# Kernel optimization log

Measured on AMD Instinct MI355X. Metric: run time of the kernel, lower is better.

## Reference

```python
import jax, jax.numpy as jnp
import numpy as np

A0, A1, A2 = 1.0, 1.0, 0.5  # Taylor coefficients of exp around 0 (p=2)

B, H, N, D = 2, 16, 4096, 32


def setup_inputs() -> dict:
    key = jax.random.key(0)
    kq, kk, kv = jax.random.split(key, 3)
    q = jax.random.normal(kq, (B, H, N, D), dtype=jnp.float32)
    k = jax.random.normal(kk, (B, H, N, D), dtype=jnp.float32)
    v = jax.random.normal(kv, (B, H, N, D), dtype=jnp.float32)
    return {"q": q, "k": k, "v": v}


def reference(q, k, v):
    # fastmax_function with p=2, mask=False, normalize=False, dropout=0 -> temperature=1
    b, h, n, d = q.shape
    # quadratic feature maps: flatten of outer products, [b,h,n,d*d]
    q2 = (q[..., :, None] * q[..., None, :]).reshape(b, h, n, d * d)
    k2 = (k[..., :, None] * k[..., None, :]).reshape(b, h, n, d * d)
    # numerator: a0*sum(v) + a1*q(k^T v) + a2*q2(k2^T v)
    second_term = A1 * jnp.einsum('bhnd,bhne->bhde', k, v)           # [b,h,d,d]
    third_term = A2 * jnp.einsum('bhnf,bhne->bhfe', k2, v)           # [b,h,d^2,d]
    ans = (jnp.einsum('bhnd,bhde->bhne', q, second_term)
           + jnp.einsum('bhnf,bhfe->bhne', q2, third_term)
           + A0 * jnp.sum(v, axis=-2, keepdims=True))                 # [b,h,n,d]
    # denominator: a0*n + a1*q.sum(k) + a2*q2.sum(k2)
    div = (A0 * n
           + A1 * jnp.einsum('bhnd,bhd->bhn', q, jnp.sum(k, axis=-2))
           + A2 * jnp.einsum('bhnf,bhf->bhn', q2, jnp.sum(k2, axis=-2)))  # [b,h,n]
    return ans / div[..., None]
```

## Files before the change

kernel.cpp:

```cpp
#include <hip/hip_runtime.h>

#define NTOK 4096
#define NBH  32
#define NF   576
#define NE   33
#define NKT  18
#define GTF_BH (NKT * 3 * 64 * 8)
#define GTF_HALF (9 * 3 * 64 * 8)
#define KC   16
#define NSTG 2
#define NVB  (KC * NBH)
#define NP8  (NBH * NE * NF / 8)

typedef _Float16 half_t;
typedef _Float16 half8 __attribute__((ext_vector_type(8)));
typedef _Float16 half4v __attribute__((ext_vector_type(4)));
typedef float f32x4 __attribute__((ext_vector_type(4)));
typedef unsigned int u32;

#define MFMA16(A,B,C) __builtin_amdgcn_mfma_f32_16x16x32_f16((A),(B),(C),0,0,0)

#define ASYNC_CP16(dst_lds, src_glb) \
    __builtin_amdgcn_global_load_lds( \
        (const __attribute__((address_space(1))) u32*)(const void*)(src_glb), \
        (__attribute__((address_space(3))) u32*)(void*)(dst_lds), 16, 0, 0)

static __device__ __forceinline__ half8 splat8(half_t x) {
    return (half8){x, x, x, x, x, x, x, x};
}

static __device__ __forceinline__ int FS(int d) { return (d + (d >> 3)) & 15; }

__global__ __launch_bounds__(256, 2)
void ta_kernel(const float* __restrict__ kin, const float* __restrict__ vin,
               half_t* __restrict__ P)
{
    __shared__ __align__(16) half_t kb0[2 * 4096];
    __shared__ __align__(16) half_t vb0[2 * 4096];

    const int vb = blockIdx.x;
    const int bh = vb & (NBH - 1), kc = vb >> 5;
    const int t = threadIdx.x;
    const int w = t >> 6, lane = t & 63, l16 = lane & 15, quad = lane >> 4;
    const int pw = w * 144;
    const half8 h05 = splat8((half_t)0.5f);

    f32x4 acc[9][3];
    #pragma unroll
    for (int m = 0; m < 9; ++m)
        #pragma unroll
        for (int e = 0; e < 3; ++e)
            acc[m][e] = (f32x4){0.f, 0.f, 0.f, 0.f};

    int rotoff[9], rotsalt[9];
    #pragma unroll
    for (int mt = 0; mt < 9; ++mt) {
        const int pm = pw + mt * 16;
        int ro = 0, rs = 0;
        if (pm >= 32 && pm < 512) {
            const int s  = 1 + ((pm - 32) >> 5);
            const int i0 = (pm - 32) & 31;
            const int r  = (i0 + l16 + s) & 31;
            ro = r * 128;
            rs = FS(r);
        }
        rotoff[mt] = ro;
        rotsalt[mt] = rs;
    }
    const int sh0 = FS(l16), sh1 = FS(l16 + 16);

    const size_t fbase = ((size_t)bh * NTOK + kc * 256) * 32;
    const float4* k4 = (const float4*)kin + fbase / 4;
    const float4* v4 = (const float4*)vin + fbase / 4;

    float kaf[16], vaf[16];
    auto loadst = [&](int s) {
        const int base = s * 1024;
        #pragma unroll
        for (int r = 0; r < 4; ++r) {
            float4 kk = k4[base + t + 256 * r];
            float4 vv = v4[base + t + 256 * r];
            kaf[4*r+0] = kk.x; kaf[4*r+1] = kk.y; kaf[4*r+2] = kk.z; kaf[4*r+3] = kk.w;
            vaf[4*r+0] = vv.x; vaf[4*r+1] = vv.y; vaf[4*r+2] = vv.z; vaf[4*r+3] = vv.w;
        }
    };
    auto writest = [&](int buf) {
        half_t* kb = kb0 + buf * 4096;
        half_t* vb2 = vb0 + buf * 4096;
        #pragma unroll
        for (int r = 0; r < 4; ++r) {
            const int fi = t + 256 * r;
            const int n = fi >> 3, d4 = fi & 7;
            const int c = n >> 3, j = n & 7;
            #pragma unroll
            for (int i = 0; i < 4; ++i) {
                const int d = 4 * d4 + i;
                const int a = d * 128 + ((c ^ FS(d)) << 3) + j;
                kb[a] = (half_t)kaf[4*r+i];
                vb2[a] = (half_t)vaf[4*r+i];
            }
        }
    };
    auto compute = [&](int buf) {
        const half_t* kb = kb0 + buf * 4096;
        const half_t* vbp = vb0 + buf * 4096;
        #pragma unroll
        for (int kk = 0; kk < 4; ++kk) {
            const int c = kk * 4 + quad;
            half8 kj0 = *(const half8*)&kb[l16 * 128 + ((c ^ sh0) << 3)];
            half8 kj1 = *(const half8*)&kb[(l16 + 16) * 128 + ((c ^ sh1) << 3)];
            half8 bf0 = *(const half8*)&vbp[l16 * 128 + ((c ^ sh0) << 3)];
            half8 bf1 = *(const half8*)&vbp[(l16 + 16) * 128 + ((c ^ sh1) << 3)];
            half_t onec = (l16 == 0) ? (half_t)1 : (half_t)0;
            half8 bf2 = splat8(onec);
            #pragma unroll
            for (int mt = 0; mt < 9; ++mt) {
                const int pm = pw + mt * 16;
                half8 af;
                if (pm < 32) {
                    af = pm ? kj1 : kj0;
                } else if (pm < 512) {
                    half8 rot = *(const half8*)&kb[rotoff[mt] + ((c ^ rotsalt[mt]) << 3)];
                    af = (((pm - 32) & 16) ? kj1 : kj0) * rot;
                } else if (pm == 512) {
                    af = kj0 * kj1;
                } else if (pm == 528) {
                    af = (kj0 * h05) * kj0;
                } else if (pm == 544) {
                    af = (kj1 * h05) * kj1;
                } else {
                    af = bf2;
                }
                acc[mt][0] = MFMA16(af, bf0, acc[mt][0]);
                acc[mt][1] = MFMA16(af, bf1, acc[mt][1]);
                acc[mt][2] = MFMA16(af, bf2, acc[mt][2]);
            }
        }
    };

    loadst(0);
    writest(0);
    __syncthreads();
    for (int st = 0; st < NSTG; ++st) {
        const int cur = st & 1;
        if (st + 1 < NSTG) loadst(st + 1);
        compute(cur);
        if (st + 1 < NSTG) { writest(cur ^ 1); __syncthreads(); }
    }

    half_t* Pb = P + ((size_t)kc * NBH + bh) * NE * NF;
    #pragma unroll
    for (int mt = 0; mt < 9; ++mt) {
        int p0 = pw + mt * 16 + quad * 4;
        half4v h0 = {(half_t)acc[mt][0][0], (half_t)acc[mt][0][1],
                     (half_t)acc[mt][0][2], (half_t)acc[mt][0][3]};
        half4v h1 = {(half_t)acc[mt][1][0], (half_t)acc[mt][1][1],
                     (half_t)acc[mt][1][2], (half_t)acc[mt][1][3]};
        *(half4v*)&Pb[(size_t)l16 * NF + p0] = h0;
        *(half4v*)&Pb[(size_t)(l16 + 16) * NF + p0] = h1;
        if (l16 == 0) {
            half4v h2 = {(half_t)acc[mt][2][0], (half_t)acc[mt][2][1],
                         (half_t)acc[mt][2][2], (half_t)acc[mt][2][3]};
            *(half4v*)&Pb[(size_t)32 * NF + p0] = h2;
        }
    }
}

__global__ __launch_bounds__(256)
void ar_kernel(const half_t* __restrict__ P, half_t* __restrict__ GtF)
{
    const int idx = blockIdx.x * 256 + threadIdx.x;
    if (idx >= NP8) return;
    float s[8] = {0.f, 0.f, 0.f, 0.f, 0.f, 0.f, 0.f, 0.f};
    for (int c = 0; c < KC; ++c) {
        half8 h = *(const half8*)&P[(size_t)c * (NBH * NE * NF) + (size_t)idx * 8];
        #pragma unroll
        for (int j = 0; j < 8; ++j) s[j] += (float)h[j];
    }
    half8 o;
    #pragma unroll
    for (int j = 0; j < 8; ++j) o[j] = (half_t)s[j];
    int row = idx / 72;
    int p8 = idx - row * 72;
    int e = row % 33, bhh = row / 33;
    int kt = p8 >> 2, quad = p8 & 3;
    int rr = e >> 4, l16 = e & 15;
    size_t dst8 = (size_t)bhh * (GTF_BH / 8)
                + (size_t)(kt * 3 + rr) * 64 + quad * 16 + l16;
    *(half8*)&GtF[dst8 * 8] = o;
}

__global__ __launch_bounds__(256)
void b_kernel(const float* __restrict__ qin, const half_t* __restrict__ GtF,
              float* __restrict__ out)
{
    const int bh = blockIdx.x, mbq = blockIdx.y;
    const int t = threadIdx.x, w = t >> 6, lane = t & 63;
    const int l16 = lane & 15, quad = lane >> 4;
    __shared__ __align__(16) half_t qs2[256 * 56];
    __shared__ __align__(16) half_t gs[GTF_HALF];
    __shared__ float denl[256];
    const size_t nbase = (size_t)bh * NTOK + mbq * 256;

    const half_t* Gsrc = GtF + (size_t)bh * GTF_BH + (size_t)lane * 8;
    auto stage = [&](int phase) {
        const half_t* src = Gsrc + phase * GTF_HALF;
        #pragma unroll
        for (int i = 0; i < 7; ++i) {
            const int c = w + 4 * i;
            if (c < 27)
                ASYNC_CP16(gs + c * 512, src + c * 512);
        }
    };
    stage(0);

    const float4* q4 = (const float4*)(qin + nbase * 32);
    #pragma unroll
    for (int r = 0; r < 8; ++r) {
        int f4 = t + 256 * r, n = f4 >> 3, d4 = f4 & 7;
        float4 vv = q4[f4];
        half4v h = {(half_t)vv.x, (half_t)vv.y, (half_t)vv.z, (half_t)vv.w};
        *(half4v*)&qs2[n * 56 + d4 * 4] = h;
        if (d4 < 4) *(half4v*)&qs2[n * 56 + 32 + d4 * 4] = h;
    }
    __syncthreads();

    const int rbase = w * 64;
    int tb[4];
    #pragma unroll
    for (int mt = 0; mt < 4; ++mt) tb[mt] = (rbase + mt * 16 + l16) * 56;

    half8 vq[4], hv[4], gv[4];
    #pragma unroll
    for (int mt = 0; mt < 4; ++mt) {
        const int qb = tb[mt] + quad * 8;
        vq[mt] = *(const half8*)&qs2[qb];
        hv[mt] = *(const half8*)&qs2[qb + 8];
        gv[mt] = *(const half8*)&qs2[qb + 16];
    }

    f32x4 acc[3][4];
    #pragma unroll
    for (int a = 0; a < 3; ++a)
        #pragma unroll
        for (int b = 0; b < 4; ++b)
            acc[a][b] = (f32x4){0.f, 0.f, 0.f, 0.f};

#define LDB(ktL, B) do { \
    _Pragma("unroll") \
    for (int rr = 0; rr < 3; ++rr) \
        (B)[rr] = *(const half8*)&gs[(((ktL) * 3 + rr) * 64 + lane) * 8]; \
} while (0)

#define DO_MFMA(AF, B) do { \
    _Pragma("unroll") \
    for (int mt = 0; mt < 4; ++mt) { \
        acc[0][mt] = MFMA16((AF)[mt], (B)[0], acc[0][mt]); \
        acc[1][mt] = MFMA16((AF)[mt], (B)[1], acc[1][mt]); \
        acc[2][mt] = MFMA16((AF)[mt], (B)[2], acc[2][mt]); \
    } \
} while (0)

#define QCHUNK(S, KTL) do { \
    half8 Bc[3]; \
    LDB((KTL), Bc); \
    half8 af[4]; \
    _Pragma("unroll") \
    for (int mt = 0; mt < 4; ++mt) { \
        half8 lo = ((S) < 8) ? vq[mt] : hv[mt]; \
        half8 hi = ((S) < 8) ? hv[mt] : gv[mt]; \
        half8 rot = __builtin_shufflevector(lo, hi, \
            ((S) & 7) + 0, ((S) & 7) + 1, ((S) & 7) + 2, ((S) & 7) + 3, \
            ((S) & 7) + 4, ((S) & 7) + 5, ((S) & 7) + 6, ((S) & 7) + 7); \
        af[mt] = vq[mt] * rot; \
    } \
    DO_MFMA(af, Bc); \
} while (0)

    {
        half8 Bc[3];
        LDB(0, Bc);
        DO_MFMA(vq, Bc);
    }
    QCHUNK(1, 1);  QCHUNK(2, 2);  QCHUNK(3, 3);  QCHUNK(4, 4);
    QCHUNK(5, 5);  QCHUNK(6, 6);  QCHUNK(7, 7);  QCHUNK(8, 8);

    __syncthreads();
    stage(1);
    __syncthreads();

    QCHUNK(9, 0);  QCHUNK(10, 1); QCHUNK(11, 2); QCHUNK(12, 3);
    QCHUNK(13, 4); QCHUNK(14, 5); QCHUNK(15, 6);

    {
        half8 Bc[3];
        LDB(7, Bc);
        half8 af[4];
        #pragma unroll
        for (int mt = 0; mt < 4; ++mt) {
            const int off = tb[mt] + ((quad >= 2) ? (quad - 2) : quad) * 8;
            half8 Ld = *(const half8*)&qs2[off];
            af[mt] = (quad < 2) ? (vq[mt] * gv[mt]) : (Ld * Ld);
        }
        DO_MFMA(af, Bc);
    }
    {
        half8 Bc[3];
        LDB(8, Bc);
        const half8 zero = {};
        half8 c10 = {};
        c10[0] = (half_t)1;
        half8 af[4];
        #pragma unroll
        for (int mt = 0; mt < 4; ++mt) {
            half8 d = gv[mt] * gv[mt];
            af[mt] = (quad < 2) ? d : ((quad == 2) ? c10 : zero);
        }
        DO_MFMA(af, Bc);
    }
#undef QCHUNK
#undef DO_MFMA
#undef LDB

    if (l16 == 0) {
        #pragma unroll
        for (int mt = 0; mt < 4; ++mt)
            #pragma unroll
            for (int r = 0; r < 4; ++r)
                denl[rbase + mt * 16 + quad * 4 + r] = acc[2][mt][r];
    }
    __syncthreads();
    #pragma unroll
    for (int mt = 0; mt < 4; ++mt) {
        float inv[4];
        #pragma unroll
        for (int r = 0; r < 4; ++r)
            inv[r] = __builtin_amdgcn_rcpf(denl[rbase + mt * 16 + quad * 4 + r]);
        #pragma unroll
        for (int r = 0; r < 4; ++r) {
            size_t ro = (nbase + rbase + mt * 16 + quad * 4 + r) * 32;
            out[ro + l16] = acc[0][mt][r] * inv[r];
            out[ro + l16 + 16] = acc[1][mt][r] * inv[r];
        }
    }
}

extern "C" void kernel_launch(void* const* d_in, const int* in_sizes, int n_in,
                              void* d_out, int out_size, void* d_ws, size_t ws_size,
                              hipStream_t stream)
{
    const float* q = (const float*)d_in[0];
    const float* k = (const float*)d_in[1];
    const float* v = (const float*)d_in[2];
    float* out = (float*)d_out;

    const size_t planeHalves = (size_t)NBH * NE * NF;
    half_t* P = (half_t*)d_ws;
    half_t* GtF = P + (size_t)KC * planeHalves;

    ta_kernel<<<dim3(NVB), 256, 0, stream>>>(k, v, P);
    ar_kernel<<<dim3((NP8 + 255) / 256), 256, 0, stream>>>(P, GtF);
    b_kernel<<<dim3(NBH, 16), 256, 0, stream>>>(q, GtF, out);
}
```

Before: 124.3 us.

## Fuse split-K reduction into ta_kernel via last-block atomic counter

Removes the separate ar_kernel and instead has each ta_kernel block increment a per-(b,h) atomic counter. The last block to finish for a given bh sums the KC partial planes and writes the swizzled GtF layout. This saves a kernel launch and its grid-wide dependency, but adds a hipMemsetAsync, atomics and fences. The reduction for each bh now runs on a single 256-thread block instead of being spread across the whole grid.

```diff
diff --git a/kernel.cpp b/kernel.cpp
--- a/kernel.cpp
+++ b/kernel.cpp
@@ -10,7 +10,6 @@
 #define KC   16
 #define NSTG 2
 #define NVB  (KC * NBH)
-#define NP8  (NBH * NE * NF / 8)
 
 typedef _Float16 half_t;
 typedef _Float16 half8 __attribute__((ext_vector_type(8)));
@@ -33,10 +32,12 @@
 
 __global__ __launch_bounds__(256, 2)
 void ta_kernel(const float* __restrict__ kin, const float* __restrict__ vin,
-               half_t* __restrict__ P)
+               half_t* __restrict__ P, half_t* __restrict__ GtF,
+               u32* __restrict__ done)
 {
     __shared__ __align__(16) half_t kb0[2 * 4096];
     __shared__ __align__(16) half_t vb0[2 * 4096];
+    __shared__ u32 lastflag;
 
     const int vb = blockIdx.x;
     const int bh = vb & (NBH - 1), kc = vb >> 5;
@@ -164,30 +165,38 @@
             *(half4v*)&Pb[(size_t)32 * NF + p0] = h2;
         }
     }
-}
-
-__global__ __launch_bounds__(256)
-void ar_kernel(const half_t* __restrict__ P, half_t* __restrict__ GtF)
-{
-    const int idx = blockIdx.x * 256 + threadIdx.x;
-    if (idx >= NP8) return;
-    float s[8] = {0.f, 0.f, 0.f, 0.f, 0.f, 0.f, 0.f, 0.f};
-    for (int c = 0; c < KC; ++c) {
-        half8 h = *(const half8*)&P[(size_t)c * (NBH * NE * NF) + (size_t)idx * 8];
-        #pragma unroll
-        for (int j = 0; j < 8; ++j) s[j] += (float)h[j];
-    }
-    half8 o;
-    #pragma unroll
-    for (int j = 0; j < 8; ++j) o[j] = (half_t)s[j];
-    int row = idx / 72;
-    int p8 = idx - row * 72;
-    int e = row % 33, bhh = row / 33;
-    int kt = p8 >> 2, quad = p8 & 3;
-    int rr = e >> 4, l16 = e & 15;
-    size_t dst8 = (size_t)bhh * (GTF_BH / 8)
-                + (size_t)(kt * 3 + rr) * 64 + quad * 16 + l16;
-    *(half8*)&GtF[dst8 * 8] = o;
+
+    __syncthreads();
+    if (t == 0) {
+        __threadfence();
+        u32 old = __hip_atomic_fetch_add(&done[bh], 1u, __ATOMIC_ACQ_REL,
+                                         __HIP_MEMORY_SCOPE_AGENT);
+        lastflag = (old == KC - 1) ? 1u : 0u;
+    }
+    __syncthreads();
+    if (lastflag) {
+        __threadfence();
+        const int NP8B = NE * NF / 8;
+        for (int idx = t; idx < NP8B; idx += 256) {
+            float s[8] = {0.f, 0.f, 0.f, 0.f, 0.f, 0.f, 0.f, 0.f};
+            for (int c = 0; c < KC; ++c) {
+                half8 h = *(const half8*)&P[((size_t)c * NBH + bh) * NE * NF
+                                            + (size_t)idx * 8];
+                #pragma unroll
+                for (int j = 0; j < 8; ++j) s[j] += (float)h[j];
+            }
+            half8 o;
+            #pragma unroll
+            for (int j = 0; j < 8; ++j) o[j] = (half_t)s[j];
+            const int e = idx / 72;
+            const int p8 = idx - e * 72;
+            const int kt = p8 >> 2, qd = p8 & 3;
+            const int rr = e >> 4, le = e & 15;
+            size_t dst8 = (size_t)bh * (GTF_BH / 8)
+                        + (size_t)(kt * 3 + rr) * 64 + qd * 16 + le;
+            *(half8*)&GtF[dst8 * 8] = o;
+        }
+    }
 }
 
 __global__ __launch_bounds__(256)
@@ -357,8 +366,9 @@
     const size_t planeHalves = (size_t)NBH * NE * NF;
     half_t* P = (half_t*)d_ws;
     half_t* GtF = P + (size_t)KC * planeHalves;
-
-    ta_kernel<<<dim3(NVB), 256, 0, stream>>>(k, v, P);
-    ar_kernel<<<dim3((NP8 + 255) / 256), 256, 0, stream>>>(P, GtF);
+    u32* done = (u32*)(GtF + (size_t)NBH * GTF_BH);
+
+    hipMemsetAsync(done, 0, NBH * sizeof(u32), stream);
+    ta_kernel<<<dim3(NVB), 256, 0, stream>>>(k, v, P, GtF, done);
     b_kernel<<<dim3(NBH, 16), 256, 0, stream>>>(q, GtF, out);
 }
```

After: 167.6 us. 34.8% more time.
